# Kernel tuning notes

Measured on AMD Instinct MI355X. Metric: run time of the kernel, lower is better.

## Reference

```python
import jax, jax.numpy as jnp
import numpy as np

B, S, DM = 4, 4096, 1024
H, DH = 16, 64          # num_attention_heads, attention_head_size
K = 128                 # Linformer projection dim (k_dims)


def setup_inputs() -> dict:
    key = jax.random.key(0)
    ks = jax.random.split(key, 9)
    s = 1.0 / np.sqrt(DM)
    return {
        "hidden_states": jax.random.normal(ks[0], (B, S, DM), jnp.float32),
        "Wq": jax.random.normal(ks[1], (DM, DM), jnp.float32) * s,
        "bq": jax.random.normal(ks[2], (DM,), jnp.float32) * 0.02,
        "Wk": jax.random.normal(ks[3], (DM, DM), jnp.float32) * s,
        "bk": jax.random.normal(ks[4], (DM,), jnp.float32) * 0.02,
        "Wv": jax.random.normal(ks[5], (DM, DM), jnp.float32) * s,
        "bv": jax.random.normal(ks[6], (DM,), jnp.float32) * 0.02,
        # E, D: [k_dims, max_input_len], init randn/sqrt(k_dims) as in torch module
        "E": jax.random.normal(ks[7], (K, S), jnp.float32) / np.sqrt(K),
        "D": jax.random.normal(ks[8], (K, S), jnp.float32) / np.sqrt(K),
    }


def reference(hidden_states, Wq, bq, Wk, bk, Wv, bv, E, D):
    b, s, _ = hidden_states.shape

    def heads(x):  # [b,s,DM] -> [b,H,s,DH]
        return x.reshape(b, s, H, DH).transpose(0, 2, 1, 3)

    # torch Linear: y = x @ W.T + b
    q = heads(hidden_states @ Wq.T + bq)   # [b,H,s,DH]
    k = heads(hidden_states @ Wk.T + bk)   # [b,H,s,DH]
    v = heads(hidden_states @ Wv.T + bv)   # [b,H,s,DH]

    # Linformer low-rank projection along the sequence axis
    pk = jnp.einsum('ks,bhsd->bhkd', E[:, :s], k)  # [b,H,K,DH]
    pv = jnp.einsum('ks,bhsd->bhkd', D[:, :s], v)  # [b,H,K,DH]

    scores = jnp.einsum('bhsd,bhkd->bhsk', q, pk) / np.sqrt(DH).astype(np.float32)
    probs = jax.nn.softmax(scores, axis=-1)        # [b,H,s,K]
    ctx = jnp.einsum('bhsk,bhkd->bhsd', probs, pv) # [b,H,s,DH]
    return ctx.transpose(0, 2, 1, 3).reshape(b, s, H * DH)
```

## Files before the change

### kernel.cpp

```cpp
#include <hip/hip_runtime.h>
#include <hip/hip_bf16.h>
#include <stdint.h>


typedef __attribute__((ext_vector_type(8))) _Float16 f16x8;
typedef __attribute__((ext_vector_type(4))) _Float16 f16x4;
typedef __attribute__((ext_vector_type(4))) float    f32x4;

__device__ __forceinline__ f32x4 mfma16(f16x8 a, f16x8 b, f32x4 c) {
    return __builtin_amdgcn_mfma_f32_16x16x32_f16(a, b, c, 0, 0, 0);
}

__device__ __forceinline__ void gload16(const void* g, void* l) {
    __builtin_amdgcn_global_load_lds(
        (const __attribute__((address_space(1))) void*)g,
        (__attribute__((address_space(3))) void*)l, 16, 0, 0);
}

__global__ __launch_bounds__(256) void prep_all(
    const float* __restrict__ hs, _Float16* __restrict__ hsB,
    const float* __restrict__ Wq, _Float16* __restrict__ WqB,
    const float* __restrict__ Wk, _Float16* __restrict__ WkH, _Float16* __restrict__ WkL,
    const float* __restrict__ Wv, _Float16* __restrict__ WvH, _Float16* __restrict__ WvL,
    const float* __restrict__ Em, _Float16* __restrict__ EB,
    const float* __restrict__ Dm, _Float16* __restrict__ DB,
    float* __restrict__ sE, float* __restrict__ sD,
    float* __restrict__ EHf) {
    __shared__ float red[256];
    const int blk = blockIdx.x, tid = threadIdx.x;

    if (blk < 2048) {
        int i = blk * 256 + tid;
        for (; i < 4194304; i += 2048 * 256) {
            f32x4 v = reinterpret_cast<const f32x4*>(hs)[i];
            f16x4 o;
#pragma unroll
            for (int j = 0; j < 4; ++j) o[j] = (_Float16)v[j];
            reinterpret_cast<f16x4*>(hsB)[i] = o;
        }
    } else if (blk < 2304) {
        int i = (blk - 2048) * 256 + tid;
        for (; i < 262144; i += 256 * 256) {
            f32x4 v = reinterpret_cast<const f32x4*>(Wq)[i];
            f16x4 o;
#pragma unroll
            for (int j = 0; j < 4; ++j) o[j] = (_Float16)v[j];
            reinterpret_cast<f16x4*>(WqB)[i] = o;
        }
    } else if (blk < 2816) {
        const int sect = (blk - 2304) >> 8;
        const float* in = sect ? Wv : Wk;
        _Float16* hi = sect ? WvH : WkH;
        _Float16* lo = sect ? WvL : WkL;
        int i = ((blk - 2304) & 255) * 256 + tid;
        for (; i < 262144; i += 256 * 256) {
            f32x4 v = reinterpret_cast<const f32x4*>(in)[i];
            f16x4 h, l;
#pragma unroll
            for (int j = 0; j < 4; ++j) {
                _Float16 hb = (_Float16)v[j];
                h[j] = hb;
                l[j] = (_Float16)(v[j] - (float)hb);
            }
            reinterpret_cast<f16x4*>(hi)[i] = h;
            reinterpret_cast<f16x4*>(lo)[i] = l;
        }
    } else if (blk < 3072) {
        const int sect = (blk - 2816) >> 7;
        const float* in = sect ? Dm : Em;
        _Float16* out = sect ? DB : EB;
        int i = ((blk - 2816) & 127) * 256 + tid;
        for (; i < 131072; i += 128 * 256) {
            f32x4 v = reinterpret_cast<const f32x4*>(in)[i];
            f16x4 o;
#pragma unroll
            for (int j = 0; j < 4; ++j) o[j] = (_Float16)v[j];
            reinterpret_cast<f16x4*>(out)[i] = o;
        }
    } else if (blk < 3328) {
        const int rb = blk - 3072;
        const float* src = (rb < 128) ? Em : Dm;
        float* dst = (rb < 128) ? sE : sD;
        const int row = rb & 127;
        float s = 0.f;
        for (int i = tid; i < 4096; i += 256) s += src[(size_t)row * 4096 + i];
        red[tid] = s;
        __syncthreads();
        for (int off = 128; off > 0; off >>= 1) {
            if (tid < off) red[tid] += red[tid + off];
            __syncthreads();
        }
        if (tid == 0) dst[row] = red[0];
    } else {
        int i = (blk - 3328) * 256 + tid;
        reinterpret_cast<f32x4*>(EHf)[i] = (f32x4)0.0f;
    }
}

__global__ __launch_bounds__(256, 4) void gemm_q_f16(
    const _Float16* __restrict__ A, const _Float16* __restrict__ B,
    const float* __restrict__ bias, _Float16* __restrict__ Q) {
    const int Kd = 1024, N = 1024, NT = 16;
    __shared__ _Float16 Asm[128 * 64];
    __shared__ _Float16 Bsm[128 * 64];
    const int tid = threadIdx.x, lane = tid & 63, wave = tid >> 6;
    const int l15 = lane & 15, lg = lane >> 4;
    const int row0 = blockIdx.x * 128, col0 = blockIdx.y * 128;
    const int wr = (wave >> 1) * 64, wc = (wave & 1) * 64;
    f32x4 acc[4][4];
#pragma unroll
    for (int m = 0; m < 4; ++m)
#pragma unroll
        for (int n = 0; n < 4; ++n) acc[m][n] = (f32x4)0.0f;

    const _Float16* aSrc[4];
    const _Float16* bSrc[4];
    int ub[4];
#pragma unroll
    for (int it = 0; it < 4; ++it) {
        int u = it * 256 + tid;
        int r = u >> 3, c = u & 7;
        int sc = (c ^ (r & 7)) * 8;
        aSrc[it] = A + (size_t)(row0 + r) * Kd + sc;
        bSrc[it] = B + (size_t)(col0 + r) * Kd + sc;
        ub[it] = it * 256 + wave * 64;
    }

#pragma unroll 1
    for (int t = 0; t < NT; ++t) {
        __syncthreads();
        const int k0 = t * 64;
#pragma unroll
        for (int it = 0; it < 4; ++it)
            gload16(aSrc[it] + k0, &Asm[ub[it] * 8]);
#pragma unroll
        for (int it = 0; it < 4; ++it)
            gload16(bSrc[it] + k0, &Bsm[ub[it] * 8]);
        asm volatile("s_waitcnt vmcnt(0)" ::: "memory");
        __syncthreads();
#pragma unroll
        for (int kk = 0; kk < 2; ++kk) {
            const int ksw = ((kk * 4 + lg) ^ (l15 & 7)) * 8;
            f16x8 af[4], bfr[4];
#pragma unroll
            for (int m = 0; m < 4; ++m)
                af[m] = *reinterpret_cast<const f16x8*>(
                    &Asm[(wr + m * 16 + l15) * 64 + ksw]);
#pragma unroll
            for (int n = 0; n < 4; ++n)
                bfr[n] = *reinterpret_cast<const f16x8*>(
                    &Bsm[(wc + n * 16 + l15) * 64 + ksw]);
#pragma unroll
            for (int m = 0; m < 4; ++m)
#pragma unroll
                for (int n = 0; n < 4; ++n) acc[m][n] = mfma16(af[m], bfr[n], acc[m][n]);
        }
    }
#pragma unroll
    for (int m = 0; m < 4; ++m)
#pragma unroll
        for (int n = 0; n < 4; ++n) {
            int colg = col0 + wc + n * 16 + l15;
            float bi = bias[colg];
#pragma unroll
            for (int r = 0; r < 4; ++r) {
                int rowg = row0 + wr + m * 16 + lg * 4 + r;
                Q[(size_t)rowg * N + colg] = (_Float16)(acc[m][n][r] + bi);
            }
        }
}

__global__ __launch_bounds__(256) void eproj2(const _Float16* __restrict__ EB,
                                              const _Float16* __restrict__ DB,
                                              const _Float16* __restrict__ X,
                                              float* __restrict__ EHf,
                                              float* __restrict__ DHf) {
    __shared__ _Float16 Ea[128 * 72];
    __shared__ _Float16 BT[128 * 72];
    const int tid = threadIdx.x, lane = tid & 63, wave = tid >> 6;
    const int l15 = lane & 15, lg = lane >> 4;
    const int sc = blockIdx.x;
    const int n0 = blockIdx.y * 128;
    const int bb = blockIdx.z & 3;
    const _Float16* Emat = (blockIdx.z >> 2) ? DB : EB;
    float* Of = (blockIdx.z >> 2) ? DHf : EHf;
    const int wr = (wave >> 1) * 64, wc = (wave & 1) * 64;
    const int nb = tid & 31, sb = tid >> 5;
    f32x4 acc[4][4];
#pragma unroll
    for (int m = 0; m < 4; ++m)
#pragma unroll
        for (int n = 0; n < 4; ++n) acc[m][n] = (f32x4)0.0f;

    for (int ks = 0; ks < 1024; ks += 64) {
        const int s0 = sc * 1024 + ks;
        __syncthreads();
#pragma unroll
        for (int i = 0; i < 4; ++i) {
            int u = tid + 256 * i;
            int r = u >> 3, c8 = (u & 7) * 8;
            *reinterpret_cast<f16x8*>(&Ea[r * 72 + c8]) =
                *reinterpret_cast<const f16x8*>(Emat + (size_t)r * 4096 + s0 + c8);
        }
        {
            f16x4 rr[8];
#pragma unroll
            for (int i = 0; i < 8; ++i)
                rr[i] = *reinterpret_cast<const f16x4*>(
                    X + (size_t)(bb * 4096 + s0 + sb * 8 + i) * 1024 + n0 + nb * 4);
#pragma unroll
            for (int j = 0; j < 4; ++j) {
                f16x8 w;
#pragma unroll
                for (int i = 0; i < 8; ++i) w[i] = rr[i][j];
                *reinterpret_cast<f16x8*>(&BT[(nb * 4 + j) * 72 + sb * 8]) = w;
            }
        }
        __syncthreads();
#pragma unroll
        for (int kk = 0; kk < 2; ++kk) {
            f16x8 af[4], bfr[4];
#pragma unroll
            for (int m = 0; m < 4; ++m)
                af[m] = *reinterpret_cast<const f16x8*>(
                    &Ea[(wr + m * 16 + l15) * 72 + kk * 32 + lg * 8]);
#pragma unroll
            for (int n = 0; n < 4; ++n)
                bfr[n] = *reinterpret_cast<const f16x8*>(
                    &BT[(wc + n * 16 + l15) * 72 + kk * 32 + lg * 8]);
#pragma unroll
            for (int m = 0; m < 4; ++m)
#pragma unroll
                for (int n = 0; n < 4; ++n) acc[m][n] = mfma16(af[m], bfr[n], acc[m][n]);
        }
    }
#pragma unroll
    for (int m = 0; m < 4; ++m)
#pragma unroll
        for (int n = 0; n < 4; ++n)
#pragma unroll
            for (int r = 0; r < 4; ++r)
                atomicAdd(&Of[(size_t)(bb * 128 + wr + m * 16 + lg * 4 + r) * 1024 +
                              n0 + wc + n * 16 + l15],
                          acc[m][n][r]);
}

__global__ __launch_bounds__(256) void gemm_split2(
    const float* __restrict__ A0, const _Float16* __restrict__ Bh0,
    const _Float16* __restrict__ Bl0, const float* __restrict__ bias0,
    const float* __restrict__ rs0, _Float16* __restrict__ PKH,
    const float* __restrict__ A1, const _Float16* __restrict__ Bh1,
    const _Float16* __restrict__ Bl1, const float* __restrict__ bias1,
    const float* __restrict__ rs1, _Float16* __restrict__ PVT) {
    const int Kd = 1024;
    const float* A = blockIdx.z ? A1 : A0;
    const _Float16* Bh = blockIdx.z ? Bh1 : Bh0;
    const _Float16* Bl = blockIdx.z ? Bl1 : Bl0;
    const float* bias = blockIdx.z ? bias1 : bias0;
    const float* rowscale = blockIdx.z ? rs1 : rs0;
    __shared__ _Float16 Ah[64 * 40], Al[64 * 40], Bhs[64 * 40], Bls[64 * 40];
    const int tid = threadIdx.x, lane = tid & 63, wave = tid >> 6;
    const int l15 = lane & 15, lg = lane >> 4;
    const int row0 = blockIdx.x * 64, col0 = blockIdx.y * 64;
    const int wr = (wave >> 1) * 32, wc = (wave & 1) * 32;
    f32x4 acc[2][2];
#pragma unroll
    for (int m = 0; m < 2; ++m)
#pragma unroll
        for (int n = 0; n < 2; ++n) acc[m][n] = (f32x4)0.0f;

    const int r = tid >> 2, c8 = (tid & 3) * 8;
    for (int k0 = 0; k0 < Kd; k0 += 32) {
        __syncthreads();
        {
            const float* src = A + (size_t)(row0 + r) * Kd + k0 + c8;
            f32x4 v0 = *reinterpret_cast<const f32x4*>(src);
            f32x4 v1 = *reinterpret_cast<const f32x4*>(src + 4);
            f16x8 h8, l8;
#pragma unroll
            for (int j = 0; j < 4; ++j) {
                _Float16 hb = (_Float16)v0[j];
                h8[j] = hb; l8[j] = (_Float16)(v0[j] - (float)hb);
            }
#pragma unroll
            for (int j = 0; j < 4; ++j) {
                _Float16 hb = (_Float16)v1[j];
                h8[4 + j] = hb; l8[4 + j] = (_Float16)(v1[j] - (float)hb);
            }
            *reinterpret_cast<f16x8*>(&Ah[r * 40 + c8]) = h8;
            *reinterpret_cast<f16x8*>(&Al[r * 40 + c8]) = l8;
            *reinterpret_cast<f16x8*>(&Bhs[r * 40 + c8]) =
                *reinterpret_cast<const f16x8*>(Bh + (size_t)(col0 + r) * Kd + k0 + c8);
            *reinterpret_cast<f16x8*>(&Bls[r * 40 + c8]) =
                *reinterpret_cast<const f16x8*>(Bl + (size_t)(col0 + r) * Kd + k0 + c8);
        }
        __syncthreads();
        f16x8 ah[2], al[2], bh[2], bl[2];
#pragma unroll
        for (int m = 0; m < 2; ++m) {
            ah[m] = *reinterpret_cast<const f16x8*>(&Ah[(wr + m * 16 + l15) * 40 + lg * 8]);
            al[m] = *reinterpret_cast<const f16x8*>(&Al[(wr + m * 16 + l15) * 40 + lg * 8]);
        }
#pragma unroll
        for (int n = 0; n < 2; ++n) {
            bh[n] = *reinterpret_cast<const f16x8*>(&Bhs[(wc + n * 16 + l15) * 40 + lg * 8]);
            bl[n] = *reinterpret_cast<const f16x8*>(&Bls[(wc + n * 16 + l15) * 40 + lg * 8]);
        }
#pragma unroll
        for (int m = 0; m < 2; ++m)
#pragma unroll
            for (int n = 0; n < 2; ++n) {
                acc[m][n] = mfma16(ah[m], bh[n], acc[m][n]);
                acc[m][n] = mfma16(al[m], bh[n], acc[m][n]);
                acc[m][n] = mfma16(ah[m], bl[n], acc[m][n]);
            }
    }
#pragma unroll
    for (int m = 0; m < 2; ++m)
#pragma unroll
        for (int n = 0; n < 2; ++n) {
            int colg = col0 + wc + n * 16 + l15;
            float bi = bias[colg];
#pragma unroll
            for (int rr2 = 0; rr2 < 4; ++rr2) {
                int rowg = row0 + wr + m * 16 + lg * 4 + rr2;
                float val = acc[m][n][rr2] + rowscale[rowg & 127] * bi;
                if (blockIdx.z == 0) {
                    PKH[(size_t)rowg * 1024 + colg] = (_Float16)(val * 0.125f);
                } else {
                    PVT[(size_t)((rowg >> 7) * 16 + (colg >> 6)) * 8192 +
                        (colg & 63) * 128 + (rowg & 127)] = (_Float16)val;
                }
            }
        }
}

__global__ __launch_bounds__(256, 4) void attn_fused(
    const _Float16* __restrict__ QH, const _Float16* __restrict__ PKH,
    const _Float16* __restrict__ PVT, float* __restrict__ Out) {
    __shared__ _Float16 smem[16384];
    const int tid = threadIdx.x, lane = tid & 63, wave = tid >> 6;
    const int l15 = lane & 15, lg = lane >> 4;
    const int st = blockIdx.x, h = blockIdx.y, bb = blockIdx.z;

    {
        const _Float16* pkh_g = PKH + (size_t)(bb * 128) * 1024 + h * 64;
        const _Float16* pvt_g = PVT + (size_t)(bb * 16 + h) * 8192;
        const int su = wave * 64 + lane;
#pragma unroll
        for (int it = 0; it < 4; ++it) {
            int u = it * 256 + su;
            int ub = it * 256 + wave * 64;
            {
                int r = u >> 3, c = u & 7;
                int sc = (c ^ (r & 7)) * 8;
                gload16(pkh_g + (size_t)r * 1024 + sc, &smem[ub * 8]);
            }
            {
                int r = u >> 4, c = u & 15;
                int sc = (c ^ (r & 7)) * 8;
                gload16(pvt_g + r * 128 + sc, &smem[8192 + ub * 8]);
            }
        }
    }
    const int srow0 = bb * 4096 + st * 128 + wave * 32;
    f16x8 qf[2][2];
#pragma unroll
    for (int m = 0; m < 2; ++m)
#pragma unroll
        for (int kk = 0; kk < 2; ++kk)
            qf[m][kk] = *reinterpret_cast<const f16x8*>(
                QH + (size_t)(srow0 + m * 16 + l15) * 1024 + h * 64 + kk * 32 + lg * 8);
    __syncthreads();

    f32x4 accT[8][2];
#pragma unroll
    for (int n = 0; n < 8; ++n)
#pragma unroll
        for (int m = 0; m < 2; ++m) accT[n][m] = (f32x4)0.0f;
#pragma unroll
    for (int kk = 0; kk < 2; ++kk)
#pragma unroll
        for (int n = 0; n < 8; ++n) {
            f16x8 pk = *reinterpret_cast<const f16x8*>(
                &smem[(n * 16 + l15) * 64 + (((kk * 4 + lg) ^ (l15 & 7)) * 8)]);
#pragma unroll
            for (int m = 0; m < 2; ++m)
                accT[n][m] = mfma16(pk, qf[m][kk], accT[n][m]);
        }
    __syncthreads();

#pragma unroll
    for (int m = 0; m < 2; ++m) {
        float v = -1e30f;
#pragma unroll
        for (int n = 0; n < 8; ++n)
#pragma unroll
            for (int r = 0; r < 4; ++r) v = fmaxf(v, accT[n][m][r]);
        v = fmaxf(v, __shfl_xor(v, 16));
        v = fmaxf(v, __shfl_xor(v, 32));
        float s = 0.f;
#pragma unroll
        for (int n = 0; n < 8; ++n)
#pragma unroll
            for (int r = 0; r < 4; ++r) {
                float e = __expf(accT[n][m][r] - v);
                accT[n][m][r] = e;
                s += e;
            }
        s += __shfl_xor(s, 16);
        s += __shfl_xor(s, 32);
        float inv = 1.0f / s;
#pragma unroll
        for (int n = 0; n < 8; ++n)
#pragma unroll
            for (int r = 0; r < 4; ++r) accT[n][m][r] *= inv;
    }

    _Float16* pw = smem + wave * 2048;
    f32x4 o[2][4];
#pragma unroll
    for (int m = 0; m < 2; ++m)
#pragma unroll
        for (int n = 0; n < 4; ++n) o[m][n] = (f32x4)0.0f;
#pragma unroll
    for (int half = 0; half < 2; ++half) {
#pragma unroll
        for (int nl = 0; nl < 4; ++nl) {
            int n = half * 4 + nl;
#pragma unroll
            for (int m = 0; m < 2; ++m) {
                int q = l15 + 16 * m;
                int kp = (nl * 8 + lg * 2) ^ ((q & 7) << 2);
                f16x4 v;
#pragma unroll
                for (int r = 0; r < 4; ++r) v[r] = (_Float16)accT[n][m][r];
                *reinterpret_cast<f16x4*>(&pw[q * 64 + kp * 2]) = v;
            }
        }
#pragma unroll
        for (int ksl = 0; ksl < 2; ++ksl) {
            f16x8 pa[2];
#pragma unroll
            for (int m = 0; m < 2; ++m) {
                int q = m * 16 + l15;
                int kpb = (ksl * 16 + lg * 4) ^ ((q & 7) << 2);
                pa[m] = *reinterpret_cast<const f16x8*>(&pw[q * 64 + kpb * 2]);
            }
            int ks = half * 2 + ksl;
#pragma unroll
            for (int n = 0; n < 4; ++n) {
                int dd = n * 16 + l15;
                f16x8 bv = *reinterpret_cast<const f16x8*>(
                    &smem[8192 + dd * 128 + (((ks * 4 + lg) ^ (dd & 7)) * 8)]);
#pragma unroll
                for (int m = 0; m < 2; ++m) o[m][n] = mfma16(pa[m], bv, o[m][n]);
            }
        }
    }

#pragma unroll
    for (int m = 0; m < 2; ++m)
#pragma unroll
        for (int n = 0; n < 4; ++n)
#pragma unroll
            for (int r = 0; r < 4; ++r) {
                int row = srow0 + m * 16 + lg * 4 + r;
                Out[(size_t)row * 1024 + h * 64 + n * 16 + l15] = o[m][n][r];
            }
}

extern "C" void kernel_launch(void* const* d_in, const int* in_sizes, int n_in,
                              void* d_out, int out_size, void* d_ws, size_t ws_size,
                              hipStream_t stream) {
    const float* hs = (const float*)d_in[0];
    const float* Wq = (const float*)d_in[1];
    const float* bq = (const float*)d_in[2];
    const float* Wk = (const float*)d_in[3];
    const float* bk = (const float*)d_in[4];
    const float* Wv = (const float*)d_in[5];
    const float* bv = (const float*)d_in[6];
    const float* Em = (const float*)d_in[7];
    const float* Dm = (const float*)d_in[8];
    float* out = (float*)d_out;
    char* ws = (char*)d_ws;

    _Float16* hsB = (_Float16*)(ws + 0);
    _Float16* WqB = (_Float16*)(ws + 33554432);
    _Float16* WkH = (_Float16*)(ws + 35651584);
    _Float16* WkL = (_Float16*)(ws + 37748736);
    _Float16* WvH = (_Float16*)(ws + 39845888);
    _Float16* WvL = (_Float16*)(ws + 41943040);
    _Float16* EB  = (_Float16*)(ws + 44040192);
    _Float16* DB  = (_Float16*)(ws + 45088768);
    float* sE  = (float*)(ws + 46137344);
    float* sD  = (float*)(ws + 46137856);
    _Float16* QHq = (_Float16*)(ws + 46138368);
    float* EHf = (float*)(ws + 113247232);
    float* DHf = (float*)(ws + 115344384);
    _Float16* PKH = (_Float16*)(ws + 117441536);
    _Float16* PVT = (_Float16*)(ws + 118490112);

    prep_all<<<4352, 256, 0, stream>>>(hs, hsB, Wq, WqB, Wk, WkH, WkL,
                                       Wv, WvH, WvL, Em, EB, Dm, DB, sE, sD,
                                       EHf);
    gemm_q_f16<<<dim3(128, 8), 256, 0, stream>>>(hsB, WqB, bq, QHq);
    eproj2<<<dim3(4, 8, 8), 256, 0, stream>>>(EB, DB, hsB, EHf, DHf);
    gemm_split2<<<dim3(8, 16, 2), 256, 0, stream>>>(EHf, WkH, WkL, bk, sE, PKH,
                                                    DHf, WvH, WvL, bv, sD, PVT);
    attn_fused<<<dim3(32, 16, 4), 256, 0, stream>>>(QHq, PKH, PVT, out);
}
```

Baseline: 151.8 us.

## Process two query tiles per attention block and async-load E tile via LDS DMA

The attention kernel now handles 256 query rows per block in two 128-row passes. This halves the grid and reuses the PK/PV tiles staged in shared memory, and it prefetches the second Q tile while the first is computed. The per-wave probability staging uses a separate smaller swizzled LDS region, so the syncthreads between score and PV phases is removed. In eproj2 the E/D tile is loaded with direct global-to-LDS loads into an unpadded, XOR-swizzled layout instead of going through registers. The cost is more LDS per attention block and fewer blocks, which may reduce parallelism.

```diff
diff --git a/kernel.cpp b/kernel.cpp
--- a/kernel.cpp
+++ b/kernel.cpp
@@ -175,11 +175,11 @@
                                               const _Float16* __restrict__ X,
                                               float* __restrict__ EHf,
                                               float* __restrict__ DHf) {
-    __shared__ _Float16 Ea[128 * 72];
+    __shared__ _Float16 Ea[128 * 64];
     __shared__ _Float16 BT[128 * 72];
     const int tid = threadIdx.x, lane = tid & 63, wave = tid >> 6;
     const int l15 = lane & 15, lg = lane >> 4;
-    const int sc = blockIdx.x;
+    const int kc = blockIdx.x;
     const int n0 = blockIdx.y * 128;
     const int bb = blockIdx.z & 3;
     const _Float16* Emat = (blockIdx.z >> 2) ? DB : EB;
@@ -192,16 +192,23 @@
 #pragma unroll
         for (int n = 0; n < 4; ++n) acc[m][n] = (f32x4)0.0f;
 
+    const _Float16* eaSrc[4];
+    int ub[4];
+#pragma unroll
+    for (int it = 0; it < 4; ++it) {
+        int u = it * 256 + tid;
+        int r = u >> 3, c = u & 7;
+        int sc = (c ^ (r & 7)) * 8;
+        eaSrc[it] = Emat + (size_t)r * 4096 + sc;
+        ub[it] = it * 256 + wave * 64;
+    }
+
     for (int ks = 0; ks < 1024; ks += 64) {
-        const int s0 = sc * 1024 + ks;
-        __syncthreads();
-#pragma unroll
-        for (int i = 0; i < 4; ++i) {
-            int u = tid + 256 * i;
-            int r = u >> 3, c8 = (u & 7) * 8;
-            *reinterpret_cast<f16x8*>(&Ea[r * 72 + c8]) =
-                *reinterpret_cast<const f16x8*>(Emat + (size_t)r * 4096 + s0 + c8);
-        }
+        const int s0 = kc * 1024 + ks;
+        __syncthreads();
+#pragma unroll
+        for (int it = 0; it < 4; ++it)
+            gload16(eaSrc[it] + s0, &Ea[ub[it] * 8]);
         {
             f16x4 rr[8];
 #pragma unroll
@@ -219,11 +226,12 @@
         __syncthreads();
 #pragma unroll
         for (int kk = 0; kk < 2; ++kk) {
+            const int ksw = ((kk * 4 + lg) ^ (l15 & 7)) * 8;
             f16x8 af[4], bfr[4];
 #pragma unroll
             for (int m = 0; m < 4; ++m)
                 af[m] = *reinterpret_cast<const f16x8*>(
-                    &Ea[(wr + m * 16 + l15) * 72 + kk * 32 + lg * 8]);
+                    &Ea[(wr + m * 16 + l15) * 64 + ksw]);
 #pragma unroll
             for (int n = 0; n < 4; ++n)
                 bfr[n] = *reinterpret_cast<const f16x8*>(
@@ -338,7 +346,7 @@
 __global__ __launch_bounds__(256, 4) void attn_fused(
     const _Float16* __restrict__ QH, const _Float16* __restrict__ PKH,
     const _Float16* __restrict__ PVT, float* __restrict__ Out) {
-    __shared__ _Float16 smem[16384];
+    __shared__ _Float16 smem[20480];
     const int tid = threadIdx.x, lane = tid & 63, wave = tid >> 6;
     const int l15 = lane & 15, lg = lane >> 4;
     const int st = blockIdx.x, h = blockIdx.y, bb = blockIdx.z;
@@ -346,10 +354,9 @@
     {
         const _Float16* pkh_g = PKH + (size_t)(bb * 128) * 1024 + h * 64;
         const _Float16* pvt_g = PVT + (size_t)(bb * 16 + h) * 8192;
-        const int su = wave * 64 + lane;
 #pragma unroll
         for (int it = 0; it < 4; ++it) {
-            int u = it * 256 + su;
+            int u = it * 256 + tid;
             int ub = it * 256 + wave * 64;
             {
                 int r = u >> 3, c = u & 7;
@@ -363,111 +370,120 @@
             }
         }
     }
-    const int srow0 = bb * 4096 + st * 128 + wave * 32;
+    const size_t qrow0 = (size_t)(bb * 4096 + st * 256 + wave * 32);
     f16x8 qf[2][2];
 #pragma unroll
     for (int m = 0; m < 2; ++m)
 #pragma unroll
         for (int kk = 0; kk < 2; ++kk)
             qf[m][kk] = *reinterpret_cast<const f16x8*>(
-                QH + (size_t)(srow0 + m * 16 + l15) * 1024 + h * 64 + kk * 32 + lg * 8);
+                QH + (qrow0 + m * 16 + l15) * 1024 + h * 64 + kk * 32 + lg * 8);
     __syncthreads();
 
-    f32x4 accT[8][2];
-#pragma unroll
-    for (int n = 0; n < 8; ++n)
-#pragma unroll
-        for (int m = 0; m < 2; ++m) accT[n][m] = (f32x4)0.0f;
-#pragma unroll
-    for (int kk = 0; kk < 2; ++kk)
-#pragma unroll
-        for (int n = 0; n < 8; ++n) {
-            f16x8 pk = *reinterpret_cast<const f16x8*>(
-                &smem[(n * 16 + l15) * 64 + (((kk * 4 + lg) ^ (l15 & 7)) * 8)]);
+    _Float16* pq = smem + 16384 + wave * 1024;
+
+#pragma unroll
+    for (int t = 0; t < 2; ++t) {
+        f32x4 accT[8][2];
+#pragma unroll
+        for (int n = 0; n < 8; ++n)
+#pragma unroll
+            for (int m = 0; m < 2; ++m) accT[n][m] = (f32x4)0.0f;
+#pragma unroll
+        for (int kk = 0; kk < 2; ++kk)
+#pragma unroll
+            for (int n = 0; n < 8; ++n) {
+                f16x8 pk = *reinterpret_cast<const f16x8*>(
+                    &smem[(n * 16 + l15) * 64 + (((kk * 4 + lg) ^ (l15 & 7)) * 8)]);
+#pragma unroll
+                for (int m = 0; m < 2; ++m)
+                    accT[n][m] = mfma16(pk, qf[m][kk], accT[n][m]);
+            }
+        if (t == 0) {
 #pragma unroll
             for (int m = 0; m < 2; ++m)
-                accT[n][m] = mfma16(pk, qf[m][kk], accT[n][m]);
-        }
-    __syncthreads();
-
-#pragma unroll
-    for (int m = 0; m < 2; ++m) {
-        float v = -1e30f;
-#pragma unroll
-        for (int n = 0; n < 8; ++n)
-#pragma unroll
-            for (int r = 0; r < 4; ++r) v = fmaxf(v, accT[n][m][r]);
-        v = fmaxf(v, __shfl_xor(v, 16));
-        v = fmaxf(v, __shfl_xor(v, 32));
-        float s = 0.f;
-#pragma unroll
-        for (int n = 0; n < 8; ++n)
-#pragma unroll
-            for (int r = 0; r < 4; ++r) {
-                float e = __expf(accT[n][m][r] - v);
-                accT[n][m][r] = e;
-                s += e;
-            }
-        s += __shfl_xor(s, 16);
-        s += __shfl_xor(s, 32);
-        float inv = 1.0f / s;
-#pragma unroll
-        for (int n = 0; n < 8; ++n)
-#pragma unroll
-            for (int r = 0; r < 4; ++r) accT[n][m][r] *= inv;
-    }
-
-    _Float16* pw = smem + wave * 2048;
-    f32x4 o[2][4];
-#pragma unroll
-    for (int m = 0; m < 2; ++m)
-#pragma unroll
-        for (int n = 0; n < 4; ++n) o[m][n] = (f32x4)0.0f;
-#pragma unroll
-    for (int half = 0; half < 2; ++half) {
-#pragma unroll
-        for (int nl = 0; nl < 4; ++nl) {
-            int n = half * 4 + nl;
-#pragma unroll
-            for (int m = 0; m < 2; ++m) {
-                int q = l15 + 16 * m;
-                int kp = (nl * 8 + lg * 2) ^ ((q & 7) << 2);
-                f16x4 v;
-#pragma unroll
-                for (int r = 0; r < 4; ++r) v[r] = (_Float16)accT[n][m][r];
-                *reinterpret_cast<f16x4*>(&pw[q * 64 + kp * 2]) = v;
-            }
-        }
-#pragma unroll
-        for (int ksl = 0; ksl < 2; ++ksl) {
+#pragma unroll
+                for (int kk = 0; kk < 2; ++kk)
+                    qf[m][kk] = *reinterpret_cast<const f16x8*>(
+                        QH + (qrow0 + 128 + m * 16 + l15) * 1024 + h * 64 +
+                        kk * 32 + lg * 8);
+        }
+
+#pragma unroll
+        for (int m = 0; m < 2; ++m) {
+            float v = -1e30f;
+#pragma unroll
+            for (int n = 0; n < 8; ++n)
+#pragma unroll
+                for (int r = 0; r < 4; ++r) v = fmaxf(v, accT[n][m][r]);
+            v = fmaxf(v, __shfl_xor(v, 16));
+            v = fmaxf(v, __shfl_xor(v, 32));
+            float s = 0.f;
+#pragma unroll
+            for (int n = 0; n < 8; ++n)
+#pragma unroll
+                for (int r = 0; r < 4; ++r) {
+                    float e = __expf(accT[n][m][r] - v);
+                    accT[n][m][r] = e;
+                    s += e;
+                }
+            s += __shfl_xor(s, 16);
+            s += __shfl_xor(s, 32);
+            float inv = 1.0f / s;
+#pragma unroll
+            for (int n = 0; n < 8; ++n)
+#pragma unroll
+                for (int r = 0; r < 4; ++r) accT[n][m][r] *= inv;
+        }
+
+        f32x4 o[2][4];
+#pragma unroll
+        for (int m = 0; m < 2; ++m)
+#pragma unroll
+            for (int n = 0; n < 4; ++n) o[m][n] = (f32x4)0.0f;
+#pragma unroll
+        for (int qt = 0; qt < 4; ++qt) {
+#pragma unroll
+            for (int nl = 0; nl < 2; ++nl) {
+                int n = qt * 2 + nl;
+#pragma unroll
+                for (int m = 0; m < 2; ++m) {
+                    int q = l15 + 16 * m;
+                    int pp = (nl * 8 + lg * 2) ^ ((q & 3) << 2);
+                    f16x4 v;
+#pragma unroll
+                    for (int r = 0; r < 4; ++r) v[r] = (_Float16)accT[n][m][r];
+                    *reinterpret_cast<f16x4*>(&pq[q * 32 + pp * 2]) = v;
+                }
+            }
             f16x8 pa[2];
 #pragma unroll
             for (int m = 0; m < 2; ++m) {
                 int q = m * 16 + l15;
-                int kpb = (ksl * 16 + lg * 4) ^ ((q & 7) << 2);
-                pa[m] = *reinterpret_cast<const f16x8*>(&pw[q * 64 + kpb * 2]);
-            }
-            int ks = half * 2 + ksl;
+                int pb = (lg * 4) ^ ((q & 3) << 2);
+                pa[m] = *reinterpret_cast<const f16x8*>(&pq[q * 32 + pb * 2]);
+            }
 #pragma unroll
             for (int n = 0; n < 4; ++n) {
                 int dd = n * 16 + l15;
                 f16x8 bv = *reinterpret_cast<const f16x8*>(
-                    &smem[8192 + dd * 128 + (((ks * 4 + lg) ^ (dd & 7)) * 8)]);
+                    &smem[8192 + dd * 128 + (((qt * 4 + lg) ^ (dd & 7)) * 8)]);
 #pragma unroll
                 for (int m = 0; m < 2; ++m) o[m][n] = mfma16(pa[m], bv, o[m][n]);
             }
         }
-    }
-
-#pragma unroll
-    for (int m = 0; m < 2; ++m)
-#pragma unroll
-        for (int n = 0; n < 4; ++n)
-#pragma unroll
-            for (int r = 0; r < 4; ++r) {
-                int row = srow0 + m * 16 + lg * 4 + r;
-                Out[(size_t)row * 1024 + h * 64 + n * 16 + l15] = o[m][n][r];
-            }
+
+        const int orow0 = bb * 4096 + st * 256 + t * 128 + wave * 32;
+#pragma unroll
+        for (int m = 0; m < 2; ++m)
+#pragma unroll
+            for (int n = 0; n < 4; ++n)
+#pragma unroll
+                for (int r = 0; r < 4; ++r) {
+                    int row = orow0 + m * 16 + lg * 4 + r;
+                    Out[(size_t)row * 1024 + h * 64 + n * 16 + l15] = o[m][n][r];
+                }
+    }
 }
 
 extern "C" void kernel_launch(void* const* d_in, const int* in_sizes, int n_in,
@@ -508,5 +524,5 @@
     eproj2<<<dim3(4, 8, 8), 256, 0, stream>>>(EB, DB, hsB, EHf, DHf);
     gemm_split2<<<dim3(8, 16, 2), 256, 0, stream>>>(EHf, WkH, WkL, bk, sE, PKH,
                                                     DHf, WvH, WvL, bv, sD, PVT);
-    attn_fused<<<dim3(32, 16, 4), 256, 0, stream>>>(QHq, PKH, PVT, out);
-}
+    attn_fused<<<dim3(16, 16, 4), 256, 0, stream>>>(QHq, PKH, PVT, out);
+}
```

New measurement: 154.2 us. About the same (+1.6%).
